# Performance work log

Hardware: AMD Instinct MI355X
Metric: run time of the kernel (lower is better)

The kernel has to match this reference:

```python
import jax, jax.numpy as jnp
import numpy as np

EPS = 1e-7  # K.epsilon()


def setup_inputs() -> dict:
    key = jax.random.key(0)
    k1, k2, k3, k4, k5, k6 = jax.random.split(key, 6)
    B, S, D = 128, 1024, 256
    ATT, QDIM = 128, 128
    inp = {
        "key": jax.random.normal(k1, (B, S, D), dtype=jnp.float32),
        "query": jax.random.normal(k2, (QDIM, 1), dtype=jnp.float32),
        "mask": jax.random.randint(k3, (B, S), 0, 2, dtype=jnp.int32),
        # learned params (keras 'normal' init ~ N(0, 0.05))
        "W": 0.05 * jax.random.normal(k4, (D, ATT), dtype=jnp.float32),
        "b": 0.05 * jax.random.normal(k5, (ATT,), dtype=jnp.float32),
        "W_u": 0.05 * jax.random.normal(k6, (ATT, QDIM), dtype=jnp.float32),
    }
    return inp


def reference(key, query, mask, W, b, W_u):
    # uit = tanh(key @ W + b): (B,S,ATT)
    uit = jnp.tanh(jnp.einsum("bsd,da->bsa", key, W) + b)
    # u = W_u @ query: (ATT,1)
    u = W_u @ query
    # scores: (B,S)
    ait = jnp.einsum("bsa,a->bs", uit, u[:, 0])
    ait = jnp.exp(ait)
    ait = ait * mask.astype(jnp.float32)
    ait = ait / (jnp.sum(ait, axis=1, keepdims=True) + EPS)
    # weighted sum over sequence -> (B,D); value == key
    out = jnp.einsum("bs,bsd->bd", ait, key)
    return out
```

## Files before the change

### kernel.cpp

```cpp
#include <hip/hip_runtime.h>
#include <hip/hip_bf16.h>
#include <math.h>

#define EPS_F 1e-7f

constexpr int Bn = 128, Sn = 1024, Dn = 256, ATTn = 128, QDn = 128;
constexpr int Mn = Bn * Sn;
constexpr int BM = 128;
constexpr int NBLK = Mn / BM;
constexpr int NJ = ATTn / 16;

typedef short short8 __attribute__((ext_vector_type(8)));
typedef float f32x4  __attribute__((ext_vector_type(4)));

__device__ inline void split_bf(float f, ushort& hi, ushort& lo) {
    uint fb = __float_as_uint(f);
    hi = (ushort)(fb >> 16);
    float hf = __uint_as_float(fb & 0xffff0000u);
    float lf = f - hf;
    __hip_bfloat16 lb = __float2bfloat16(lf);
    __builtin_memcpy(&lo, &lb, 2);
}

__device__ inline float tanh_fast(float x) {
    float cx = fminf(9.0f, fmaxf(-9.0f, x));
    float e = __builtin_amdgcn_exp2f(cx * 2.8853900817779268f);
    return (e - 1.0f) * __builtin_amdgcn_rcpf(e + 1.0f);
}

__device__ inline void gload_lds16(const void* g, void* lds_base) {
    __builtin_amdgcn_global_load_lds(
        (const __attribute__((address_space(1))) unsigned int*)g,
        (__attribute__((address_space(3))) unsigned int*)lds_base, 16, 0, 0);
}

#define MFMA_BF16 __builtin_amdgcn_mfma_f32_16x16x32_bf16


__global__ __launch_bounds__(256) void k_prep(
    const float* __restrict__ Wu, const float* __restrict__ q,
    float* __restrict__ u,
    const float* __restrict__ W,
    ushort* __restrict__ Bhi)
{
    if (blockIdx.x == 0) {
        __shared__ float qs[QDn];
        int t = threadIdx.x;
        if (t < QDn) qs[t] = q[t];
        __syncthreads();
        if (t < ATTn) {
            float acc = 0.f;
            #pragma unroll 8
            for (int j = 0; j < QDn; ++j) acc += Wu[t * QDn + j] * qs[j];
            u[t] = acc;
        }
        return;
    }
    int gid  = (blockIdx.x - 1) * 256 + threadIdx.x;
    int lane = gid & 63;
    int j    = (gid >> 6) & 7;
    int ks   = gid >> 9;
    int col  = j * 16 + (lane & 15);
    int kb   = ks * 32 + (lane >> 4) * 8;
    #pragma unroll
    for (int i = 0; i < 8; ++i) {
        float f = W[(size_t)(kb + i) * ATTn + col];
        __hip_bfloat16 h = __float2bfloat16(f);
        ushort hu; __builtin_memcpy(&hu, &h, 2);
        Bhi[(size_t)gid * 8 + i] = hu;
    }
}


__device__ __forceinline__ void stage_Bq(
    float4* bbuf, const ushort* __restrict__ Bhi, int q, int t, int w)
{
    #pragma unroll
    for (int i = 0; i < 2; ++i) {
        int c = i * 512 + t;
        gload_lds16(Bhi + (size_t)(q * 1024 + c) * 8, bbuf + (i * 512 + w * 64));
    }
}

__device__ __forceinline__ void stage_A(
    float4* abuf, const float* __restrict__ key, int row0, int ks, int t, int w)
{
    #pragma unroll
    for (int i = 0; i < 2; ++i) {
        int s   = i * 512 + t;
        int row = s >> 3;
        int cl  = (s & 7) ^ (row & 7);
        const float* src = key + (size_t)(row0 + row) * Dn + ks * 32 + cl * 4;
        gload_lds16(src, abuf + (i * 512 + w * 64));
    }
}

template<int KS>
__device__ __forceinline__ void compute_ks(
    const float4* abuf, const float4* bbuf,
    f32x4 (&acc)[NJ], int w, int lane)
{
    const int l15 = lane & 15, lg = lane >> 4;
    const int r = w * 16 + l15;
    float4 a0 = abuf[r * 8 + ((lg * 2)     ^ (r & 7))];
    float4 a1 = abuf[r * 8 + ((lg * 2 + 1) ^ (r & 7))];
    short8 ah, al;
    {
        float f[8] = {a0.x, a0.y, a0.z, a0.w, a1.x, a1.y, a1.z, a1.w};
        #pragma unroll
        for (int i = 0; i < 8; ++i) {
            ushort h, l;
            split_bf(f[i], h, l);
            ah[i] = (short)h; al[i] = (short)l;
        }
    }
    const float4* Bh = bbuf + (KS & 1) * 512 + lane;
    short8 bh[3];
    bh[0] = *(const short8*)(Bh);
    bh[1] = *(const short8*)(Bh + 64);
    bh[2] = *(const short8*)(Bh + 128);
    __builtin_amdgcn_s_setprio(1);
    #pragma unroll
    for (int j = 0; j < NJ; ++j) {
        const int slot = j % 3;
        short8 cbh = bh[slot];
        if (j + 3 < NJ)
            bh[slot] = *(const short8*)(Bh + (j + 3) * 64);
        acc[j] = MFMA_BF16(ah, cbh, acc[j], 0, 0, 0);
        acc[j] = MFMA_BF16(al, cbh, acc[j], 0, 0, 0);
    }
    __builtin_amdgcn_s_setprio(0);
}

#define PIN() __builtin_amdgcn_sched_barrier(0)

__global__ __launch_bounds__(512, 4) void k_scores(
    const float*  __restrict__ key,
    const ushort* __restrict__ Bhi,
    const float*  __restrict__ bias, const float* __restrict__ u,
    const int*    __restrict__ mask,
    float* __restrict__ P, float* __restrict__ den)
{
    __shared__ float4 smem[4096];
    float4* B0 = smem;
    float4* B1 = smem + 1024;
    float4* A0 = smem + 2048;
    float4* A1 = smem + 3072;
    float*  esp   = (float*)smem;
    float4* partp = smem + 64;

    const int t    = threadIdx.x;
    const int lane = t & 63;
    const int w    = t >> 6;
    const int gb   = blockIdx.x;
    const int row0 = gb * BM;
    const int l15  = lane & 15;
    const int lg   = lane >> 4;

    f32x4 acc[NJ];
    #pragma unroll
    for (int j = 0; j < NJ; ++j) acc[j] = (f32x4){0.f, 0.f, 0.f, 0.f};

    stage_Bq(B0, Bhi, 0, t, w);
    stage_A(A0, key, row0, 0, t, w);
    __syncthreads();

    stage_Bq(B1, Bhi, 1, t, w);
    stage_A(A1, key, row0, 1, t, w);
    PIN();
    compute_ks<0>(A0, B0, acc, w, lane);
    __syncthreads();
    stage_A(A0, key, row0, 2, t, w);
    PIN();
    compute_ks<1>(A1, B0, acc, w, lane);
    __syncthreads();
    stage_Bq(B0, Bhi, 2, t, w);
    stage_A(A1, key, row0, 3, t, w);
    PIN();
    compute_ks<2>(A0, B1, acc, w, lane);
    __syncthreads();
    stage_A(A0, key, row0, 4, t, w);
    PIN();
    compute_ks<3>(A1, B1, acc, w, lane);
    __syncthreads();
    stage_Bq(B1, Bhi, 3, t, w);
    stage_A(A1, key, row0, 5, t, w);
    PIN();
    compute_ks<4>(A0, B0, acc, w, lane);
    __syncthreads();
    stage_A(A0, key, row0, 6, t, w);
    PIN();
    compute_ks<5>(A1, B0, acc, w, lane);
    __syncthreads();
    stage_A(A1, key, row0, 7, t, w);
    PIN();
    compute_ks<6>(A0, B1, acc, w, lane);
    __syncthreads();
    compute_ks<7>(A1, B1, acc, w, lane);
    __syncthreads();

    float s4[4] = {0.f, 0.f, 0.f, 0.f};
    #pragma unroll
    for (int j = 0; j < NJ; ++j) {
        int col = j * 16 + l15;
        float bv = bias[col], uvv = u[col];
        #pragma unroll
        for (int reg = 0; reg < 4; ++reg)
            s4[reg] += tanh_fast(acc[j][reg] + bv) * uvv;
    }
    #pragma unroll
    for (int reg = 0; reg < 4; ++reg) {
        float s = s4[reg];
        s += __shfl_xor(s, 1);
        s += __shfl_xor(s, 2);
        s += __shfl_xor(s, 4);
        s += __shfl_xor(s, 8);
        if (l15 == 0) {
            int rl = w * 16 + lg * 4 + reg;
            esp[rl] = __builtin_amdgcn_exp2f(s * 1.4426950408889634f)
                      * (float)mask[row0 + rl];
        }
    }
    __syncthreads();

    if (t < 64) {
        float v = esp[t] + esp[t + 64];
        #pragma unroll
        for (int m = 1; m < 64; m <<= 1) v += __shfl_xor(v, m);
        if (t == 0) den[gb] = v;
    }

    {
        const float4* kt = (const float4*)(key + (size_t)(row0 + w * 16) * Dn);
        float4 a2 = make_float4(0.f, 0.f, 0.f, 0.f);
        #pragma unroll 4
        for (int s2 = 0; s2 < 16; ++s2) {
            float wv   = esp[w * 16 + s2];
            float4 kvv = kt[(size_t)s2 * 64 + lane];
            a2.x += wv * kvv.x; a2.y += wv * kvv.y;
            a2.z += wv * kvv.z; a2.w += wv * kvv.w;
        }
        partp[w * 64 + lane] = a2;
    }
    __syncthreads();

    if (t < 64) {
        float4 o = partp[t];
        #pragma unroll
        for (int wv = 1; wv < 8; ++wv) {
            float4 p = partp[wv * 64 + t];
            o.x += p.x; o.y += p.y; o.z += p.z; o.w += p.w;
        }
        *(float4*)(P + (size_t)gb * Dn + t * 4) = o;
    }
}

__global__ __launch_bounds__(256) void k_final(const float* __restrict__ P,
        const float* __restrict__ den, float* __restrict__ out) {
    int b = blockIdx.x, t = threadIdx.x;
    float dtot = 0.f;
    #pragma unroll
    for (int k = 0; k < 8; ++k) dtot += den[b * 8 + k];
    float o = 0.f;
    #pragma unroll
    for (int k = 0; k < 8; ++k) o += P[(size_t)(b * 8 + k) * Dn + t];
    out[(size_t)b * Dn + t] = o / (dtot + EPS_F);
}

extern "C" void kernel_launch(void* const* d_in, const int* in_sizes, int n_in,
                              void* d_out, int out_size, void* d_ws, size_t ws_size,
                              hipStream_t stream) {
    const float* key   = (const float*)d_in[0];
    const float* query = (const float*)d_in[1];
    const int*   mask  = (const int*)d_in[2];
    const float* W     = (const float*)d_in[3];
    const float* bias  = (const float*)d_in[4];
    const float* Wu    = (const float*)d_in[5];
    float* out = (float*)d_out;

    char* ws = (char*)d_ws;
    float*  u   = (float*)(ws);
    ushort* Bhi = (ushort*)(ws + 512);
    float*  Pp  = (float*)(ws + 66048);
    float*  den = (float*)(ws + 1114624);

    hipLaunchKernelGGL(k_prep,   dim3(17),   dim3(256), 0, stream, Wu, query, u, W, Bhi);
    hipLaunchKernelGGL(k_scores, dim3(NBLK), dim3(512), 0, stream,
                       key, Bhi, bias, u, mask, Pp, den);
    hipLaunchKernelGGL(k_final,  dim3(Bn),   dim3(256), 0, stream, Pp, den, out);
}
```

Measured before the change: 51.90 us.

## Triple-buffer key tiles with vmcnt-counted barriers in score kernel

Adds a third LDS buffer for key tiles so global loads run two stages ahead of compute. Full __syncthreads calls become explicit s_waitcnt vmcnt(N) plus s_barrier, which wait only for the loads the next stage needs instead of draining every outstanding load. Bias and u are loaded into registers at kernel start rather than after the MFMA loop. LDS use grows from 64KB to 80KB per block, which may reduce occupancy relative to the launch-bounds target of 4 blocks, and the hand-counted vmcnt values must exactly match the number of loads issued per stage.

```diff
diff --git a/kernel.cpp b/kernel.cpp
--- a/kernel.cpp
+++ b/kernel.cpp
@@ -35,6 +35,14 @@
 }
 
 #define MFMA_BF16 __builtin_amdgcn_mfma_f32_16x16x32_bf16
+#define PIN() __builtin_amdgcn_sched_barrier(0)
+
+#define CBAR(N)                                               \
+    PIN();                                                    \
+    asm volatile("s_waitcnt vmcnt(" #N ")" ::: "memory");     \
+    PIN();                                                    \
+    __builtin_amdgcn_s_barrier();                             \
+    PIN();
 
 
 __global__ __launch_bounds__(256) void k_prep(
@@ -132,8 +140,6 @@
     __builtin_amdgcn_s_setprio(0);
 }
 
-#define PIN() __builtin_amdgcn_sched_barrier(0)
-
 __global__ __launch_bounds__(512, 4) void k_scores(
     const float*  __restrict__ key,
     const ushort* __restrict__ Bhi,
@@ -141,11 +147,12 @@
     const int*    __restrict__ mask,
     float* __restrict__ P, float* __restrict__ den)
 {
-    __shared__ float4 smem[4096];
+    __shared__ float4 smem[5120];
     float4* B0 = smem;
     float4* B1 = smem + 1024;
     float4* A0 = smem + 2048;
     float4* A1 = smem + 3072;
+    float4* A2 = smem + 4096;
     float*  esp   = (float*)smem;
     float4* partp = smem + 64;
 
@@ -157,56 +164,62 @@
     const int l15  = lane & 15;
     const int lg   = lane >> 4;
 
+    float bv[NJ], uv[NJ];
+    #pragma unroll
+    for (int j = 0; j < NJ; ++j) {
+        int col = j * 16 + l15;
+        bv[j] = bias[col]; uv[j] = u[col];
+    }
+    PIN();
+
     f32x4 acc[NJ];
     #pragma unroll
     for (int j = 0; j < NJ; ++j) acc[j] = (f32x4){0.f, 0.f, 0.f, 0.f};
 
+    stage_A(A0, key, row0, 0, t, w);
     stage_Bq(B0, Bhi, 0, t, w);
-    stage_A(A0, key, row0, 0, t, w);
-    __syncthreads();
-
+    PIN();
+    stage_A(A1, key, row0, 1, t, w);
     stage_Bq(B1, Bhi, 1, t, w);
-    stage_A(A1, key, row0, 1, t, w);
+    CBAR(4);
+
+    stage_A(A2, key, row0, 2, t, w);
     PIN();
     compute_ks<0>(A0, B0, acc, w, lane);
-    __syncthreads();
-    stage_A(A0, key, row0, 2, t, w);
+    CBAR(2);
+    stage_A(A0, key, row0, 3, t, w);
     PIN();
     compute_ks<1>(A1, B0, acc, w, lane);
-    __syncthreads();
+    CBAR(2);
+    stage_A(A1, key, row0, 4, t, w);
     stage_Bq(B0, Bhi, 2, t, w);
-    stage_A(A1, key, row0, 3, t, w);
-    PIN();
-    compute_ks<2>(A0, B1, acc, w, lane);
-    __syncthreads();
-    stage_A(A0, key, row0, 4, t, w);
-    PIN();
-    compute_ks<3>(A1, B1, acc, w, lane);
-    __syncthreads();
+    PIN();
+    compute_ks<2>(A2, B1, acc, w, lane);
+    CBAR(4);
+    stage_A(A2, key, row0, 5, t, w);
+    PIN();
+    compute_ks<3>(A0, B1, acc, w, lane);
+    CBAR(2);
+    stage_A(A0, key, row0, 6, t, w);
     stage_Bq(B1, Bhi, 3, t, w);
-    stage_A(A1, key, row0, 5, t, w);
-    PIN();
-    compute_ks<4>(A0, B0, acc, w, lane);
-    __syncthreads();
-    stage_A(A0, key, row0, 6, t, w);
-    PIN();
-    compute_ks<5>(A1, B0, acc, w, lane);
-    __syncthreads();
+    PIN();
+    compute_ks<4>(A1, B0, acc, w, lane);
+    CBAR(4);
     stage_A(A1, key, row0, 7, t, w);
     PIN();
+    compute_ks<5>(A2, B0, acc, w, lane);
+    CBAR(2);
     compute_ks<6>(A0, B1, acc, w, lane);
-    __syncthreads();
+    CBAR(0);
     compute_ks<7>(A1, B1, acc, w, lane);
     __syncthreads();
 
     float s4[4] = {0.f, 0.f, 0.f, 0.f};
     #pragma unroll
     for (int j = 0; j < NJ; ++j) {
-        int col = j * 16 + l15;
-        float bv = bias[col], uvv = u[col];
         #pragma unroll
         for (int reg = 0; reg < 4; ++reg)
-            s4[reg] += tanh_fast(acc[j][reg] + bv) * uvv;
+            s4[reg] += tanh_fast(acc[j][reg] + bv[j]) * uv[j];
     }
     #pragma unroll
     for (int reg = 0; reg < 4; ++reg) {
```

New measurement: 53.09 us. +2.3%, slower.

## Shrink LDS staging to per-k-step B tiles and raise occupancy target

Applied to the files above, without the earlier changes.

Replaces the paired-k-step B staging (two 16 KB B buffers each covering two k-steps) with one-k-step B tiles, double-buffered alongside A, cutting shared memory from 64 KB to 48 KB per block. The launch bounds minimum-blocks hint rises from 4 to 6 so more waves can be resident per CU to hide global-load latency. The hand-unrolled schedule becomes a uniform prefetch-next/compute-current loop. In exchange B is now reloaded every k-step instead of every other step, and the tighter register budget from the higher occupancy target risks spills.

```diff
diff --git a/kernel.cpp b/kernel.cpp
--- a/kernel.cpp
+++ b/kernel.cpp
@@ -35,6 +35,7 @@
 }
 
 #define MFMA_BF16 __builtin_amdgcn_mfma_f32_16x16x32_bf16
+#define PIN() __builtin_amdgcn_sched_barrier(0)
 
 
 __global__ __launch_bounds__(256) void k_prep(
@@ -72,14 +73,10 @@
 }
 
 
-__device__ __forceinline__ void stage_Bq(
-    float4* bbuf, const ushort* __restrict__ Bhi, int q, int t, int w)
-{
-    #pragma unroll
-    for (int i = 0; i < 2; ++i) {
-        int c = i * 512 + t;
-        gload_lds16(Bhi + (size_t)(q * 1024 + c) * 8, bbuf + (i * 512 + w * 64));
-    }
+__device__ __forceinline__ void stage_B8(
+    float4* bbuf, const ushort* __restrict__ Bhi, int ks, int t, int w)
+{
+    gload_lds16(Bhi + (size_t)(ks * 512 + t) * 8, bbuf + w * 64);
 }
 
 __device__ __forceinline__ void stage_A(
@@ -95,7 +92,6 @@
     }
 }
 
-template<int KS>
 __device__ __forceinline__ void compute_ks(
     const float4* abuf, const float4* bbuf,
     f32x4 (&acc)[NJ], int w, int lane)
@@ -114,7 +110,7 @@
             ah[i] = (short)h; al[i] = (short)l;
         }
     }
-    const float4* Bh = bbuf + (KS & 1) * 512 + lane;
+    const float4* Bh = bbuf + lane;
     short8 bh[3];
     bh[0] = *(const short8*)(Bh);
     bh[1] = *(const short8*)(Bh + 64);
@@ -132,20 +128,16 @@
     __builtin_amdgcn_s_setprio(0);
 }
 
-#define PIN() __builtin_amdgcn_sched_barrier(0)
-
-__global__ __launch_bounds__(512, 4) void k_scores(
+__global__ __launch_bounds__(512, 6) void k_scores(
     const float*  __restrict__ key,
     const ushort* __restrict__ Bhi,
     const float*  __restrict__ bias, const float* __restrict__ u,
     const int*    __restrict__ mask,
     float* __restrict__ P, float* __restrict__ den)
 {
-    __shared__ float4 smem[4096];
-    float4* B0 = smem;
-    float4* B1 = smem + 1024;
-    float4* A0 = smem + 2048;
-    float4* A1 = smem + 3072;
+    __shared__ float4 smem[3072];
+    float4* Bb[2] = {smem, smem + 512};
+    float4* Ab[2] = {smem + 1024, smem + 2048};
     float*  esp   = (float*)smem;
     float4* partp = smem + 64;
 
@@ -161,43 +153,20 @@
     #pragma unroll
     for (int j = 0; j < NJ; ++j) acc[j] = (f32x4){0.f, 0.f, 0.f, 0.f};
 
-    stage_Bq(B0, Bhi, 0, t, w);
-    stage_A(A0, key, row0, 0, t, w);
+    stage_A(Ab[0], key, row0, 0, t, w);
+    stage_B8(Bb[0], Bhi, 0, t, w);
     __syncthreads();
 
-    stage_Bq(B1, Bhi, 1, t, w);
-    stage_A(A1, key, row0, 1, t, w);
-    PIN();
-    compute_ks<0>(A0, B0, acc, w, lane);
-    __syncthreads();
-    stage_A(A0, key, row0, 2, t, w);
-    PIN();
-    compute_ks<1>(A1, B0, acc, w, lane);
-    __syncthreads();
-    stage_Bq(B0, Bhi, 2, t, w);
-    stage_A(A1, key, row0, 3, t, w);
-    PIN();
-    compute_ks<2>(A0, B1, acc, w, lane);
-    __syncthreads();
-    stage_A(A0, key, row0, 4, t, w);
-    PIN();
-    compute_ks<3>(A1, B1, acc, w, lane);
-    __syncthreads();
-    stage_Bq(B1, Bhi, 3, t, w);
-    stage_A(A1, key, row0, 5, t, w);
-    PIN();
-    compute_ks<4>(A0, B0, acc, w, lane);
-    __syncthreads();
-    stage_A(A0, key, row0, 6, t, w);
-    PIN();
-    compute_ks<5>(A1, B0, acc, w, lane);
-    __syncthreads();
-    stage_A(A1, key, row0, 7, t, w);
-    PIN();
-    compute_ks<6>(A0, B1, acc, w, lane);
-    __syncthreads();
-    compute_ks<7>(A1, B1, acc, w, lane);
-    __syncthreads();
+    #pragma unroll
+    for (int ks = 0; ks < 8; ++ks) {
+        if (ks + 1 < 8) {
+            stage_A(Ab[(ks + 1) & 1], key, row0, ks + 1, t, w);
+            stage_B8(Bb[(ks + 1) & 1], Bhi, ks + 1, t, w);
+        }
+        PIN();
+        compute_ks(Ab[ks & 1], Bb[ks & 1], acc, w, lane);
+        __syncthreads();
+    }
 
     float s4[4] = {0.f, 0.f, 0.f, 0.f};
     #pragma unroll
```

New measurement: 53.29 us. 2.7% more time.

## Reuse register-held bf16 key fragments for the weighted sum instead of reloading key

Applied to the files above, without the earlier changes.

Each GEMM k-step now stores the bf16 high half of its A fragment in a per-thread array. The epilogue builds the per-block weighted sum over key from those saved fragments with cross-lane shuffle reductions, rather than reading key rows from global memory again. This removes a second global/L2 read of the key tile. In exchange it adds 32 live VGPRs under a tight launch bound, which risks spills or lower occupancy, and adds many shuffles. The output now uses bf16-truncated key values instead of fp32, which lowers accuracy.

```diff
diff --git a/kernel.cpp b/kernel.cpp
--- a/kernel.cpp
+++ b/kernel.cpp
@@ -22,6 +22,10 @@
     __builtin_memcpy(&lo, &lb, 2);
 }
 
+__device__ inline float hi2f(short h) {
+    return __uint_as_float(((uint)(ushort)h) << 16);
+}
+
 __device__ inline float tanh_fast(float x) {
     float cx = fminf(9.0f, fmaxf(-9.0f, x));
     float e = __builtin_amdgcn_exp2f(cx * 2.8853900817779268f);
@@ -35,6 +39,7 @@
 }
 
 #define MFMA_BF16 __builtin_amdgcn_mfma_f32_16x16x32_bf16
+#define PIN() __builtin_amdgcn_sched_barrier(0)
 
 
 __global__ __launch_bounds__(256) void k_prep(
@@ -98,7 +103,7 @@
 template<int KS>
 __device__ __forceinline__ void compute_ks(
     const float4* abuf, const float4* bbuf,
-    f32x4 (&acc)[NJ], int w, int lane)
+    f32x4 (&acc)[NJ], short8 (&ahk)[8], int w, int lane)
 {
     const int l15 = lane & 15, lg = lane >> 4;
     const int r = w * 16 + l15;
@@ -114,6 +119,7 @@
             ah[i] = (short)h; al[i] = (short)l;
         }
     }
+    ahk[KS] = ah;
     const float4* Bh = bbuf + (KS & 1) * 512 + lane;
     short8 bh[3];
     bh[0] = *(const short8*)(Bh);
@@ -132,8 +138,6 @@
     __builtin_amdgcn_s_setprio(0);
 }
 
-#define PIN() __builtin_amdgcn_sched_barrier(0)
-
 __global__ __launch_bounds__(512, 4) void k_scores(
     const float*  __restrict__ key,
     const ushort* __restrict__ Bhi,
@@ -147,7 +151,7 @@
     float4* A0 = smem + 2048;
     float4* A1 = smem + 3072;
     float*  esp   = (float*)smem;
-    float4* partp = smem + 64;
+    float*  partp = (float*)(smem + 64);
 
     const int t    = threadIdx.x;
     const int lane = t & 63;
@@ -160,6 +164,7 @@
     f32x4 acc[NJ];
     #pragma unroll
     for (int j = 0; j < NJ; ++j) acc[j] = (f32x4){0.f, 0.f, 0.f, 0.f};
+    short8 ahk[8];
 
     stage_Bq(B0, Bhi, 0, t, w);
     stage_A(A0, key, row0, 0, t, w);
@@ -168,35 +173,35 @@
     stage_Bq(B1, Bhi, 1, t, w);
     stage_A(A1, key, row0, 1, t, w);
     PIN();
-    compute_ks<0>(A0, B0, acc, w, lane);
+    compute_ks<0>(A0, B0, acc, ahk, w, lane);
     __syncthreads();
     stage_A(A0, key, row0, 2, t, w);
     PIN();
-    compute_ks<1>(A1, B0, acc, w, lane);
+    compute_ks<1>(A1, B0, acc, ahk, w, lane);
     __syncthreads();
     stage_Bq(B0, Bhi, 2, t, w);
     stage_A(A1, key, row0, 3, t, w);
     PIN();
-    compute_ks<2>(A0, B1, acc, w, lane);
+    compute_ks<2>(A0, B1, acc, ahk, w, lane);
     __syncthreads();
     stage_A(A0, key, row0, 4, t, w);
     PIN();
-    compute_ks<3>(A1, B1, acc, w, lane);
+    compute_ks<3>(A1, B1, acc, ahk, w, lane);
     __syncthreads();
     stage_Bq(B1, Bhi, 3, t, w);
     stage_A(A1, key, row0, 5, t, w);
     PIN();
-    compute_ks<4>(A0, B0, acc, w, lane);
+    compute_ks<4>(A0, B0, acc, ahk, w, lane);
     __syncthreads();
     stage_A(A0, key, row0, 6, t, w);
     PIN();
-    compute_ks<5>(A1, B0, acc, w, lane);
+    compute_ks<5>(A1, B0, acc, ahk, w, lane);
     __syncthreads();
     stage_A(A1, key, row0, 7, t, w);
     PIN();
-    compute_ks<6>(A0, B1, acc, w, lane);
-    __syncthreads();
-    compute_ks<7>(A1, B1, acc, w, lane);
+    compute_ks<6>(A0, B1, acc, ahk, w, lane);
+    __syncthreads();
+    compute_ks<7>(A1, B1, acc, ahk, w, lane);
     __syncthreads();
 
     float s4[4] = {0.f, 0.f, 0.f, 0.f};
@@ -231,24 +236,34 @@
     }
 
     {
-        const float4* kt = (const float4*)(key + (size_t)(row0 + w * 16) * Dn);
-        float4 a2 = make_float4(0.f, 0.f, 0.f, 0.f);
-        #pragma unroll 4
-        for (int s2 = 0; s2 < 16; ++s2) {
-            float wv   = esp[w * 16 + s2];
-            float4 kvv = kt[(size_t)s2 * 64 + lane];
-            a2.x += wv * kvv.x; a2.y += wv * kvv.y;
-            a2.z += wv * kvv.z; a2.w += wv * kvv.w;
-        }
-        partp[w * 64 + lane] = a2;
+        float e = esp[w * 16 + l15];
+        #pragma unroll
+        for (int ks = 0; ks < 8; ++ks) {
+            float p[8];
+            #pragma unroll
+            for (int i = 0; i < 8; ++i)
+                p[i] = e * hi2f(ahk[ks][i]);
+            #pragma unroll
+            for (int i = 0; i < 8; ++i) {
+                p[i] += __shfl_xor(p[i], 1);
+                p[i] += __shfl_xor(p[i], 2);
+                p[i] += __shfl_xor(p[i], 4);
+                p[i] += __shfl_xor(p[i], 8);
+            }
+            if (l15 == 0) {
+                float* dst = &partp[w * 256 + ks * 32 + lg * 8];
+                *(float4*)(dst)     = make_float4(p[0], p[1], p[2], p[3]);
+                *(float4*)(dst + 4) = make_float4(p[4], p[5], p[6], p[7]);
+            }
+        }
     }
     __syncthreads();
 
     if (t < 64) {
-        float4 o = partp[t];
+        float4 o = *(float4*)&partp[t * 4];
         #pragma unroll
         for (int wv = 1; wv < 8; ++wv) {
-            float4 p = partp[wv * 64 + t];
+            float4 p = *(float4*)&partp[wv * 256 + t * 4];
             o.x += p.x; o.y += p.y; o.z += p.z; o.w += p.w;
         }
         *(float4*)(P + (size_t)gb * Dn + t * 4) = o;
```

New measurement: 61.88 us. +19.2%, slower.
